# Performance work log

Measured on AMD Instinct MI355X. Metric: run time of the kernel, lower is better.

The kernel has to match this reference:

```python
import jax, jax.numpy as jnp
import numpy as np

D_MODEL = 256
NHEAD = 8
D_K = D_MODEL // NHEAD
IM_SIZE = 8
SCALE = float(IM_SIZE ** 2)  # sqrt(im_size**4)


def setup_inputs() -> dict:
    key = jax.random.key(0)
    ks = jax.random.split(key, 9)
    B, P, S = 8, 256, 8
    s = 1.0 / np.sqrt(D_MODEL)
    return {
        "x": jax.random.normal(ks[0], (B, P, S, S, D_MODEL), jnp.float32),
        "Wq": jax.random.normal(ks[1], (D_MODEL, D_MODEL), jnp.float32) * s,
        "bq": jax.random.normal(ks[2], (D_MODEL,), jnp.float32) * s,
        "Wk": jax.random.normal(ks[3], (D_MODEL, D_MODEL), jnp.float32) * s,
        "bk": jax.random.normal(ks[4], (D_MODEL,), jnp.float32) * s,
        "Wv": jax.random.normal(ks[5], (D_MODEL, D_MODEL), jnp.float32) * s,
        "bv": jax.random.normal(ks[6], (D_MODEL,), jnp.float32) * s,
        "Wo": jax.random.normal(ks[7], (D_MODEL, D_MODEL), jnp.float32) * s,
        "bo": jax.random.normal(ks[8], (D_MODEL,), jnp.float32) * s,
    }


def _split_heads(t):
    # torch: view(..., d_k, nhead).permute(0,5,1,2,3,4) -> [b, n, p, x, y, d_k]
    b, p, sx, sy, _ = t.shape
    t = t.reshape(b, p, sx, sy, D_K, NHEAD)
    return jnp.transpose(t, (0, 5, 1, 2, 3, 4))


def reference(x, Wq, bq, Wk, bk, Wv, bv, Wo, bo):
    Q = _split_heads(x @ Wq.T + bq)
    K = _split_heads(x @ Wk.T + bk)
    V = _split_heads(x @ Wv.T + bv)
    # scores over flattened (x, y, d_k) dims
    scores = jnp.einsum('bnpxyd,bnqxyd->bnpq', Q, K) / SCALE
    attn = jax.nn.softmax(scores, axis=-1)
    out = jnp.einsum('bnpq,bnqxyd->bnpxyd', attn, V)
    # permute to [b, p, x, y, d_k, n] then merge (d_k, n) -> d_model
    out = jnp.transpose(out, (0, 2, 3, 4, 5, 1))
    b, p, sx, sy, _, _ = out.shape
    out = out.reshape(b, p, sx, sy, NHEAD * D_K)
    return out @ Wo.T + bo
```

## Files before the change

### kernel.cpp

```cpp
#include <hip/hip_runtime.h>
#include <hip/hip_bf16.h>


typedef __bf16 bf16;
typedef __attribute__((ext_vector_type(8))) __bf16 bf16x8;
typedef __attribute__((ext_vector_type(4))) float floatx4;
typedef __attribute__((ext_vector_type(8))) unsigned short ushort8;

#define CDIM 2048

static __device__ __forceinline__ floatx4 mfma16(bf16x8 a, bf16x8 b, floatx4 c) {
  return __builtin_amdgcn_mfma_f32_16x16x32_bf16(a, b, c, 0, 0, 0);
}

static __device__ __forceinline__ void gload_lds16(const void* g, void* l) {
  __builtin_amdgcn_global_load_lds((const __attribute__((address_space(1))) void*)g,
                                   (__attribute__((address_space(3))) void*)l, 16, 0, 0);
}

__global__ __launch_bounds__(256) void k0_prep(
    const float* __restrict__ Wq, const float* __restrict__ bq,
    const float* __restrict__ Wk, const float* __restrict__ bk,
    const float* __restrict__ Wv, const float* __restrict__ bv,
    const float* __restrict__ Wo,
    bf16* __restrict__ Wp, bf16* __restrict__ Wk3, float* __restrict__ biasp)
{
  const int bid = blockIdx.x, tid = threadIdx.x;
  int g = (bid & 31) * 256 + tid;
  int lane = g & 63, rowblk = (g >> 6) & 15, kk = g >> 10;
  int h = lane >> 4, cl = lane & 15;
  int d0 = kk * 32 + 8 * h;
  if (bid < 32) {
    int ip = rowblk * 16 + cl;
    int isrc = ((ip & 31) << 3) | (ip >> 5);
#pragma unroll
    for (int mat = 0; mat < 3; mat++) {
      const float* W = (mat == 0) ? Wq : (mat == 1) ? Wk : Wv;
      bf16x8 v;
#pragma unroll
      for (int j = 0; j < 8; j++) v[j] = (bf16)W[isrc * 256 + d0 + j];
      *reinterpret_cast<bf16x8*>(Wp + ((size_t)mat * 8192 + g) * 8) = v;
    }
    if (bid == 0 && tid < 256) {
      int bs = ((tid & 31) << 3) | (tid >> 5);
      biasp[tid] = bq[bs]; biasp[256 + tid] = bk[bs]; biasp[512 + tid] = bv[bs];
    }
  } else {
    int j = rowblk * 16 + cl;
    bf16x8 v;
#pragma unroll
    for (int jj = 0; jj < 8; jj++) {
      int c = d0 + jj;
      v[jj] = (bf16)Wo[j * 256 + (((c & 31) << 3) | (c >> 5))];
    }
    *reinterpret_cast<bf16x8*>(Wk3 + (size_t)g * 8) = v;
  }
}

__global__ __launch_bounds__(512, 4) void k1_qkv(
    const float* __restrict__ x, const bf16* __restrict__ Wp,
    const float* __restrict__ biasp,
    bf16* __restrict__ Qs, bf16* __restrict__ Ks, bf16* __restrict__ Vt)
{
  __shared__ bf16 buf[2][64 * 256];
  const int bx = blockIdx.x;
  const int tid = threadIdx.x;
  const int lane = tid & 63;
  const int w = tid >> 6;
  const int h = lane >> 4, cl = lane & 15;
  const int c7 = cl & 7;

  floatx4 sreg[8];

#define K1_LOAD(VB)                                                          \
  {                                                                          \
    int a_ = (VB) / 24;                                                      \
    int t0_ = (a_ * 8 + ((VB) & 7)) * 64;                                    \
    _Pragma("unroll")                                                        \
    for (int k = 0; k < 4; ++k) {                                            \
      int G = k * 512 + tid;                                                 \
      int row = G >> 5;                                                      \
      const float* sp = x + (size_t)(t0_ + row) * 256 + (G & 31) * 8;        \
      sreg[2 * k]     = *reinterpret_cast<const floatx4*>(sp);               \
      sreg[2 * k + 1] = *reinterpret_cast<const floatx4*>(sp + 4);           \
    }                                                                        \
  }

#define K1_CVTWRITE(BUFI)                                                    \
  {                                                                          \
    _Pragma("unroll")                                                        \
    for (int k = 0; k < 4; ++k) {                                            \
      int G = k * 512 + tid;                                                 \
      int row = G >> 5;                                                      \
      bf16x8 v;                                                              \
      _Pragma("unroll")                                                      \
      for (int j = 0; j < 4; j++) {                                          \
        v[j] = (bf16)sreg[2 * k][j];                                         \
        v[4 + j] = (bf16)sreg[2 * k + 1][j];                                 \
      }                                                                      \
      int Gp = (G & ~7) | ((G ^ row) & 7);                                   \
      *reinterpret_cast<bf16x8*>(&buf[BUFI][Gp * 8]) = v;                    \
    }                                                                        \
  }

#define K1_COMPUTE(VB, BUFI)                                                 \
  {                                                                          \
    int a_ = (VB) / 24;                                                      \
    int rem_ = (VB) - a_ * 24;                                               \
    int mat_ = rem_ >> 3;                                                    \
    int t0_ = (a_ * 8 + (rem_ & 7)) * 64;                                    \
    const bf16* Wm = Wp + (size_t)mat_ * 65536;                              \
    floatx4 acc[4][2];                                                       \
    _Pragma("unroll")                                                        \
    for (int i = 0; i < 4; i++)                                              \
      _Pragma("unroll")                                                      \
      for (int j = 0; j < 2; j++) acc[i][j] = (floatx4)0.0f;                 \
    _Pragma("unroll 2")                                                      \
    for (int kk = 0; kk < 8; ++kk) {                                         \
      bf16x8 av[4];                                                          \
      _Pragma("unroll")                                                      \
      for (int mt = 0; mt < 4; mt++) {                                       \
        int rr = mt * 16 + cl;                                               \
        int G = rr * 32 + kk * 4 + h;                                        \
        int Gp = (G & ~7) | ((G ^ c7) & 7);                                  \
        av[mt] = *reinterpret_cast<const bf16x8*>(&buf[BUFI][Gp * 8]);       \
      }                                                                      \
      bf16x8 b0 = *reinterpret_cast<const bf16x8*>(                          \
          Wm + ((size_t)(kk * 16 + w * 2 + 0) * 64 + lane) * 8);             \
      bf16x8 b1 = *reinterpret_cast<const bf16x8*>(                          \
          Wm + ((size_t)(kk * 16 + w * 2 + 1) * 64 + lane) * 8);             \
      _Pragma("unroll")                                                      \
      for (int mt = 0; mt < 4; mt++) acc[mt][0] = mfma16(av[mt], b0, acc[mt][0]); \
      _Pragma("unroll")                                                      \
      for (int mt = 0; mt < 4; mt++) acc[mt][1] = mfma16(av[mt], b1, acc[mt][1]); \
    }                                                                        \
    int b_ = t0_ >> 14;                                                      \
    int p_ = (t0_ >> 6) & 255;                                               \
    if (mat_ < 2) {                                                          \
      bf16* ob = ((mat_ == 0) ? Qs : Ks) + ((size_t)(b_ * 8 + w) * 256 + p_) * 2048; \
      _Pragma("unroll")                                                      \
      for (int nt = 0; nt < 2; nt++) {                                       \
        const int ip = w * 32 + nt * 16 + cl;                                \
        const float bb = biasp[mat_ * 256 + ip];                             \
        const int dk = nt * 16 + cl;                                         \
        _Pragma("unroll")                                                    \
        for (int mt = 0; mt < 4; mt++)                                       \
          _Pragma("unroll")                                                  \
          for (int r = 0; r < 4; r++) {                                      \
            int sxy = mt * 16 + 4 * h + r;                                   \
            ob[sxy * 32 + dk] = (bf16)(acc[mt][nt][r] + bb);                 \
          }                                                                  \
      }                                                                      \
    } else {                                                                 \
      _Pragma("unroll")                                                      \
      for (int nt = 0; nt < 2; nt++) {                                       \
        const int ip = w * 32 + nt * 16 + cl;                                \
        const float bb = biasp[512 + ip];                                    \
        _Pragma("unroll")                                                    \
        for (int mt = 0; mt < 4; mt++)                                       \
          _Pragma("unroll")                                                  \
          for (int r = 0; r < 4; r++) {                                      \
            int t = t0_ + mt * 16 + 4 * h + r;                               \
            Vt[(size_t)t * 256 + ip] = (bf16)(acc[mt][nt][r] + bb);          \
          }                                                                  \
      }                                                                      \
    }                                                                        \
  }

  K1_LOAD(bx);
  K1_CVTWRITE(0);
  __syncthreads();
#pragma unroll
  for (int u = 1; u < 4; ++u) {
    K1_LOAD(bx + u * 1536);
    K1_COMPUTE(bx + (u - 1) * 1536, (u - 1) & 1);
    __syncthreads();
    K1_CVTWRITE(u & 1);
    __syncthreads();
  }
  K1_COMPUTE(bx + 3 * 1536, 1);

#undef K1_LOAD
#undef K1_CVTWRITE
#undef K1_COMPUTE
}

__global__ __launch_bounds__(1024, 1) void k2a_scores(
    const bf16* __restrict__ Qs, const bf16* __restrict__ Ks,
    bf16* __restrict__ attn)
{
  __shared__ bf16 Qch[3][128 * 64];
  __shared__ bf16 Kch[3][256 * 64];
  __shared__ float redmax[4][4][32];
  __shared__ float redsum[4][4][32];

  const int bx = blockIdx.x;
  const int bn = bx & 63;
  const int p0 = (bx >> 6) * 128;
  const int tid = threadIdx.x;
  const int lane = tid & 63;
  const int w = tid >> 6;
  const int wr = w >> 2, wc = w & 3;
  const int h = lane >> 4, cl = lane & 15;

  const bf16* Qb = Qs + (size_t)bn * 524288 + (size_t)p0 * 2048;
  const bf16* Kb = Ks + (size_t)bn * 524288;

  const int Lq = w * 64 + lane;
  const int rq = Lq >> 3, sq = (Lq & 7) ^ (rq & 7);
  const size_t qsrc = (size_t)rq * 2048 + sq * 8;
  int rk[2]; size_t ksrc[2];
#pragma unroll
  for (int i = 0; i < 2; ++i) {
    int L = i * 1024 + w * 64 + lane;
    rk[i] = L >> 3;
    int s = (L & 7) ^ (rk[i] & 7);
    ksrc[i] = (size_t)rk[i] * 2048 + s * 8;
  }

#define K2A_STAGE(bufi, c)                                                  \
  {                                                                         \
    gload_lds16(Qb + qsrc + (c) * 64, &Qch[bufi][(w * 64) * 8]);            \
    gload_lds16(Kb + ksrc[0] + (c) * 64, &Kch[bufi][(w * 64) * 8]);         \
    gload_lds16(Kb + ksrc[1] + (c) * 64, &Kch[bufi][(1024 + w * 64) * 8]);  \
  }

  floatx4 acc[2][4];
#pragma unroll
  for (int i = 0; i < 2; i++)
#pragma unroll
    for (int j = 0; j < 4; j++) acc[i][j] = (floatx4)0.0f;

  K2A_STAGE(0, 0);
  K2A_STAGE(1, 1);
  asm volatile("s_waitcnt vmcnt(3)" ::: "memory");
  __builtin_amdgcn_s_barrier();
  __builtin_amdgcn_sched_barrier(0);

  for (int c = 0; c < 32; ++c) {
    const int cur = c % 3;
    if (c + 2 < 32) { const int nb = (c + 2) % 3; K2A_STAGE(nb, c + 2); }
#pragma unroll
    for (int kk = 0; kk < 2; ++kk) {
      bf16x8 av[2], bv[4];
#pragma unroll
      for (int mt = 0; mt < 2; mt++) {
        int row = wr * 32 + mt * 16 + cl;
        int gg = kk * 4 + h;
        av[mt] = *reinterpret_cast<const bf16x8*>(
            &Qch[cur][(row * 8 + (gg ^ (row & 7))) * 8]);
      }
#pragma unroll
      for (int nt = 0; nt < 4; nt++) {
        int row = wc * 64 + nt * 16 + cl;
        int gg = kk * 4 + h;
        bv[nt] = *reinterpret_cast<const bf16x8*>(
            &Kch[cur][(row * 8 + (gg ^ (row & 7))) * 8]);
      }
#pragma unroll
      for (int nt = 0; nt < 4; nt++)
#pragma unroll
        for (int mt = 0; mt < 2; mt++)
          acc[mt][nt] = mfma16(av[mt], bv[nt], acc[mt][nt]);
    }
    if (c + 2 < 32) asm volatile("s_waitcnt vmcnt(3)" ::: "memory");
    else            asm volatile("s_waitcnt vmcnt(0)" ::: "memory");
    __builtin_amdgcn_s_barrier();
    __builtin_amdgcn_sched_barrier(0);
  }

  float pm[2][4];
#pragma unroll
  for (int mt = 0; mt < 2; mt++)
#pragma unroll
    for (int r = 0; r < 4; r++)
      pm[mt][r] = fmaxf(fmaxf(acc[mt][0][r], acc[mt][1][r]),
                        fmaxf(acc[mt][2][r], acc[mt][3][r]));
#pragma unroll
  for (int off = 1; off < 16; off <<= 1)
#pragma unroll
    for (int mt = 0; mt < 2; mt++)
#pragma unroll
      for (int r = 0; r < 4; r++)
        pm[mt][r] = fmaxf(pm[mt][r], __shfl_xor(pm[mt][r], off, 64));
  if (cl == 0) {
#pragma unroll
    for (int mt = 0; mt < 2; mt++)
#pragma unroll
      for (int r = 0; r < 4; r++) redmax[wr][wc][mt * 16 + 4 * h + r] = pm[mt][r];
  }
  __syncthreads();

  float gm[2][4], ps[2][4];
#pragma unroll
  for (int mt = 0; mt < 2; mt++)
#pragma unroll
    for (int r = 0; r < 4; r++) {
      int row = mt * 16 + 4 * h + r;
      gm[mt][r] = fmaxf(fmaxf(redmax[wr][0][row], redmax[wr][1][row]),
                        fmaxf(redmax[wr][2][row], redmax[wr][3][row]));
      ps[mt][r] = 0.0f;
    }
  const float KS = 1.44269504088896340736f / 64.0f;
#pragma unroll
  for (int mt = 0; mt < 2; mt++)
#pragma unroll
    for (int nt = 0; nt < 4; nt++)
#pragma unroll
      for (int r = 0; r < 4; r++) {
        float e = exp2f((acc[mt][nt][r] - gm[mt][r]) * KS);
        acc[mt][nt][r] = e;
        ps[mt][r] += e;
      }
#pragma unroll
  for (int off = 1; off < 16; off <<= 1)
#pragma unroll
    for (int mt = 0; mt < 2; mt++)
#pragma unroll
      for (int r = 0; r < 4; r++) ps[mt][r] += __shfl_xor(ps[mt][r], off, 64);
  if (cl == 0) {
#pragma unroll
    for (int mt = 0; mt < 2; mt++)
#pragma unroll
      for (int r = 0; r < 4; r++) redsum[wr][wc][mt * 16 + 4 * h + r] = ps[mt][r];
  }
  __syncthreads();

#pragma unroll
  for (int mt = 0; mt < 2; mt++)
#pragma unroll
    for (int r = 0; r < 4; r++) {
      int row = mt * 16 + 4 * h + r;
      float gs = (redsum[wr][0][row] + redsum[wr][1][row])
               + (redsum[wr][2][row] + redsum[wr][3][row]);
      ps[mt][r] = 1.0f / gs;
    }
#pragma unroll
  for (int nt = 0; nt < 4; nt++) {
    int q = wc * 64 + nt * 16 + cl;
#pragma unroll
    for (int mt = 0; mt < 2; mt++)
#pragma unroll
      for (int r = 0; r < 4; r++) {
        int row = p0 + wr * 32 + mt * 16 + 4 * h + r;
        attn[(size_t)bn * 65536 + row * 256 + q] = (bf16)(acc[mt][nt][r] * ps[mt][r]);
      }
  }
#undef K2A_STAGE
}

__global__ __launch_bounds__(256) void k2t_transpose(
    const bf16* __restrict__ Vtok, bf16* __restrict__ Vq)
{
  const int bx = blockIdx.x;
  const int bn = bx & 63;
  const int r2 = bx >> 6;
  const int q0 = (r2 & 3) * 64;
  const int c0 = (r2 >> 2) * 64;
  const int b = bn >> 3, n = bn & 7;
  __shared__ unsigned short tile[64][65];
  const unsigned short* src = (const unsigned short*)Vtok;
  unsigned short* dst = (unsigned short*)Vq + (size_t)bn * 524288;
  {
    const int q = threadIdx.x >> 3;
    const int cj = (threadIdx.x & 7) * 8;
    const int c = c0 + cj;
    const int sxy = c >> 5, dk0 = c & 31;
#pragma unroll
    for (int it = 0; it < 2; ++it) {
      int qq = q + it * 32;
      size_t sa = (size_t)((b * 256 + q0 + qq) * 64 + sxy) * 256 + n * 32 + dk0;
      ushort8 s = *reinterpret_cast<const ushort8*>(src + sa);
#pragma unroll
      for (int j = 0; j < 8; j++) tile[qq][cj + j] = s[j];
    }
  }
  __syncthreads();
  {
    const int crow = threadIdx.x >> 2;
    const int qj = (threadIdx.x & 3) * 8;
#pragma unroll
    for (int it = 0; it < 2; ++it) {
      int qq = qj + it * 32;
      ushort8 sv;
#pragma unroll
      for (int j = 0; j < 8; j++) sv[j] = tile[qq + j][crow];
      *reinterpret_cast<ushort8*>(dst + (size_t)(c0 + crow) * 256 + q0 + qq) = sv;
    }
  }
}

__global__ __launch_bounds__(512, 6) void k2b_pv(
    const bf16* __restrict__ attn, const bf16* __restrict__ Vq,
    bf16* __restrict__ yhat)
{
  __shared__ bf16 As[64 * 256];
  const int bx = blockIdx.x;
  const int bn = bx & 63;
  const int r2 = bx >> 6;
  const int p0 = (r2 & 3) * 64;
  const int c0 = (r2 >> 2) * 256;
  const int b = bn >> 3, n = bn & 7;
  const int tid = threadIdx.x;
  const int lane = tid & 63;
  const int w = tid >> 6;
  const int h = lane >> 4, cl = lane & 15;
  const int c7 = cl & 7;

  const bf16* Ab = attn + (size_t)bn * 65536 + (size_t)p0 * 256;
  const bf16* Vb = Vq + (size_t)bn * 524288;

#pragma unroll
  for (int i = 0; i < 4; ++i) {
    int L = (i * 8 + w) * 64 + lane;
    int S = (L & ~7) | ((L ^ (L >> 5)) & 7);
    gload_lds16(Ab + (size_t)S * 8, &As[(size_t)(i * 8 + w) * 64 * 8]);
  }
  __syncthreads();

  floatx4 acc[4][2];
#pragma unroll
  for (int i = 0; i < 4; i++)
#pragma unroll
    for (int j = 0; j < 2; j++) acc[i][j] = (floatx4)0.0f;

#pragma unroll 2
  for (int kk = 0; kk < 8; ++kk) {
    bf16x8 av[4];
#pragma unroll
    for (int mt = 0; mt < 4; mt++) {
      int rr = mt * 16 + cl;
      int G = rr * 32 + kk * 4 + h;
      int Gp = (G & ~7) | ((G ^ c7) & 7);
      av[mt] = *reinterpret_cast<const bf16x8*>(&As[Gp * 8]);
    }
    bf16x8 b0 = *reinterpret_cast<const bf16x8*>(
        Vb + (size_t)(c0 + w * 32 + cl) * 256 + kk * 32 + 8 * h);
    bf16x8 b1 = *reinterpret_cast<const bf16x8*>(
        Vb + (size_t)(c0 + w * 32 + 16 + cl) * 256 + kk * 32 + 8 * h);
#pragma unroll
    for (int mt = 0; mt < 4; mt++) acc[mt][0] = mfma16(av[mt], b0, acc[mt][0]);
#pragma unroll
    for (int mt = 0; mt < 4; mt++) acc[mt][1] = mfma16(av[mt], b1, acc[mt][1]);
  }

#pragma unroll
  for (int nt = 0; nt < 2; nt++) {
    const int cg = c0 + w * 32 + nt * 16 + cl;
    const int dk = cg & 31, sxy = cg >> 5;
#pragma unroll
    for (int mt = 0; mt < 4; mt++)
#pragma unroll
      for (int r = 0; r < 4; r++) {
        int p = p0 + mt * 16 + 4 * h + r;
        size_t t = (size_t)((b * 256 + p) * 64) + sxy;
        yhat[t * 256 + n * 32 + dk] = (bf16)acc[mt][nt][r];
      }
  }
}

__global__ __launch_bounds__(512, 6) void k3_out(
    const bf16* __restrict__ yhat, const bf16* __restrict__ Wk3,
    const float* __restrict__ bo, float* __restrict__ outp)
{
  __shared__ bf16 As[64 * 256];
  const int t0 = blockIdx.x * 64;
  const int tid = threadIdx.x;
  const int lane = tid & 63;
  const int w = tid >> 6;
  const int h = lane >> 4, cl = lane & 15;
  const int c7 = cl & 7;

  const bf16* Ab = yhat + (size_t)t0 * 256;

#pragma unroll
  for (int i = 0; i < 4; ++i) {
    int L = (i * 8 + w) * 64 + lane;
    int S = (L & ~7) | ((L ^ (L >> 5)) & 7);
    gload_lds16(Ab + (size_t)S * 8, &As[(size_t)(i * 8 + w) * 64 * 8]);
  }
  __syncthreads();

  floatx4 acc[4][2];
#pragma unroll
  for (int i = 0; i < 4; i++)
#pragma unroll
    for (int j = 0; j < 2; j++) acc[i][j] = (floatx4)0.0f;

#pragma unroll 2
  for (int kk = 0; kk < 8; ++kk) {
    bf16x8 av[4];
#pragma unroll
    for (int mt = 0; mt < 4; mt++) {
      int rr = mt * 16 + cl;
      int G = rr * 32 + kk * 4 + h;
      int Gp = (G & ~7) | ((G ^ c7) & 7);
      av[mt] = *reinterpret_cast<const bf16x8*>(&As[Gp * 8]);
    }
    bf16x8 b0 = *reinterpret_cast<const bf16x8*>(
        Wk3 + ((size_t)(kk * 16 + w * 2 + 0) * 64 + lane) * 8);
    bf16x8 b1 = *reinterpret_cast<const bf16x8*>(
        Wk3 + ((size_t)(kk * 16 + w * 2 + 1) * 64 + lane) * 8);
#pragma unroll
    for (int mt = 0; mt < 4; mt++) acc[mt][0] = mfma16(av[mt], b0, acc[mt][0]);
#pragma unroll
    for (int mt = 0; mt < 4; mt++) acc[mt][1] = mfma16(av[mt], b1, acc[mt][1]);
  }

#pragma unroll
  for (int nt = 0; nt < 2; nt++) {
    const int j = w * 32 + nt * 16 + cl;
    const float bb = bo[j];
#pragma unroll
    for (int mt = 0; mt < 4; mt++)
#pragma unroll
      for (int r = 0; r < 4; r++)
        outp[(size_t)(t0 + mt * 16 + 4 * h + r) * 256 + j] = acc[mt][nt][r] + bb;
  }
}

extern "C" void kernel_launch(void* const* d_in, const int* in_sizes, int n_in,
                              void* d_out, int out_size, void* d_ws, size_t ws_size,
                              hipStream_t stream) {
  const float* x  = (const float*)d_in[0];
  const float* Wq = (const float*)d_in[1];
  const float* bq = (const float*)d_in[2];
  const float* Wk = (const float*)d_in[3];
  const float* bk = (const float*)d_in[4];
  const float* Wv = (const float*)d_in[5];
  const float* bv = (const float*)d_in[6];
  const float* Wo = (const float*)d_in[7];
  const float* bo = (const float*)d_in[8];
  float* outp = (float*)d_out;

  char* ws = (char*)d_ws;
  const size_t SZ_QKV = 67108864;
  size_t off = 0;
  bf16* Qs   = (bf16*)(ws + off); off += SZ_QKV;
  bf16* Ks   = (bf16*)(ws + off); off += SZ_QKV;
  bf16* Vtok = (bf16*)(ws + off); off += SZ_QKV;
  bf16* attn = (bf16*)(ws + off); off += 8388608;
  bf16* Wp   = (bf16*)(ws + off); off += 393216;
  bf16* Wk3  = (bf16*)(ws + off); off += 131072;
  float* biasp = (float*)(ws + off); off += 3072;
  if (ws_size < off) return;

  bf16* yhat = Qs;
  bf16* Vq   = Ks;

  k0_prep<<<64, 256, 0, stream>>>(Wq, bq, Wk, bk, Wv, bv, Wo, Wp, Wk3, biasp);
  k1_qkv<<<1536, 512, 0, stream>>>(x, Wp, biasp, Qs, Ks, Vtok);
  k2a_scores<<<128, 1024, 0, stream>>>(Qs, Ks, attn);
  k2t_transpose<<<8192, 256, 0, stream>>>(Vtok, Vq);
  k2b_pv<<<2048, 512, 0, stream>>>(attn, Vq, yhat);
  k3_out<<<2048, 512, 0, stream>>>(yhat, Wk3, bo, outp);
}
```

Baseline: 313.1 us.

## Pin QKV weight slice in registers per block and split output columns across blocks

The QKV projection kernel now fixes each block to one projection matrix and one half of its output columns. The block's weight fragments are preloaded into registers once and reused for all four token tiles, so the inner loop no longer fetches weights from global memory at every k-step. The grid doubles to 3072 blocks and each wave computes one 16-column tile instead of two. In exchange, each x tile is now read and converted by six blocks instead of three, which leans on L2 hits to absorb the extra input traffic.

After: 328.7 us. 1.05x slower.

```diff
diff --git a/kernel.cpp b/kernel.cpp
--- a/kernel.cpp
+++ b/kernel.cpp
@@ -64,23 +64,38 @@
 {
   __shared__ bf16 buf[2][64 * 256];
   const int bx = blockIdx.x;
+  const int a0 = bx / 48;
+  const int rem = bx - a0 * 48;
+  const int mat = rem >> 4;
+  const int ch = (rem >> 3) & 1;
+  const int x8 = rem & 7;
   const int tid = threadIdx.x;
   const int lane = tid & 63;
   const int w = tid >> 6;
   const int h = lane >> 4, cl = lane & 15;
   const int c7 = cl & 7;
 
+  const bf16* Wm = Wp + (size_t)mat * 65536;
+  bf16x8 wreg[8];
+#pragma unroll
+  for (int kk = 0; kk < 8; ++kk)
+    wreg[kk] = *reinterpret_cast<const bf16x8*>(
+        Wm + ((size_t)(kk * 16 + ch * 8 + w) * 64 + lane) * 8);
+
+  const int ip = (ch * 8 + w) * 16 + cl;
+  const float bb = biasp[mat * 256 + ip];
+  const int n_ = ip >> 5, dkc = ip & 31;
+  bf16* qkout = (mat == 0) ? Qs : Ks;
+
   floatx4 sreg[8];
 
-#define K1_LOAD(VB)                                                          \
+#define K1_LOAD(T0)                                                          \
   {                                                                          \
-    int a_ = (VB) / 24;                                                      \
-    int t0_ = (a_ * 8 + ((VB) & 7)) * 64;                                    \
     _Pragma("unroll")                                                        \
     for (int k = 0; k < 4; ++k) {                                            \
       int G = k * 512 + tid;                                                 \
       int row = G >> 5;                                                      \
-      const float* sp = x + (size_t)(t0_ + row) * 256 + (G & 31) * 8;        \
+      const float* sp = x + (size_t)((T0) + row) * 256 + (G & 31) * 8;       \
       sreg[2 * k]     = *reinterpret_cast<const floatx4*>(sp);               \
       sreg[2 * k + 1] = *reinterpret_cast<const floatx4*>(sp + 4);           \
     }                                                                        \
@@ -103,19 +118,12 @@
     }                                                                        \
   }
 
-#define K1_COMPUTE(VB, BUFI)                                                 \
+#define K1_COMPUTE(T0, BUFI)                                                 \
   {                                                                          \
-    int a_ = (VB) / 24;                                                      \
-    int rem_ = (VB) - a_ * 24;                                               \
-    int mat_ = rem_ >> 3;                                                    \
-    int t0_ = (a_ * 8 + (rem_ & 7)) * 64;                                    \
-    const bf16* Wm = Wp + (size_t)mat_ * 65536;                              \
-    floatx4 acc[4][2];                                                       \
+    floatx4 acc[4];                                                          \
     _Pragma("unroll")                                                        \
-    for (int i = 0; i < 4; i++)                                              \
-      _Pragma("unroll")                                                      \
-      for (int j = 0; j < 2; j++) acc[i][j] = (floatx4)0.0f;                 \
-    _Pragma("unroll 2")                                                      \
+    for (int i = 0; i < 4; i++) acc[i] = (floatx4)0.0f;                      \
+    _Pragma("unroll")                                                        \
     for (int kk = 0; kk < 8; ++kk) {                                         \
       bf16x8 av[4];                                                          \
       _Pragma("unroll")                                                      \
@@ -125,60 +133,48 @@
         int Gp = (G & ~7) | ((G ^ c7) & 7);                                  \
         av[mt] = *reinterpret_cast<const bf16x8*>(&buf[BUFI][Gp * 8]);       \
       }                                                                      \
-      bf16x8 b0 = *reinterpret_cast<const bf16x8*>(                          \
-          Wm + ((size_t)(kk * 16 + w * 2 + 0) * 64 + lane) * 8);             \
-      bf16x8 b1 = *reinterpret_cast<const bf16x8*>(                          \
-          Wm + ((size_t)(kk * 16 + w * 2 + 1) * 64 + lane) * 8);             \
       _Pragma("unroll")                                                      \
-      for (int mt = 0; mt < 4; mt++) acc[mt][0] = mfma16(av[mt], b0, acc[mt][0]); \
+      for (int mt = 0; mt < 4; mt++)                                         \
+        acc[mt] = mfma16(av[mt], wreg[kk], acc[mt]);                         \
+    }                                                                        \
+    int b_ = (T0) >> 14;                                                     \
+    int p_ = ((T0) >> 6) & 255;                                              \
+    if (mat < 2) {                                                           \
+      bf16* ob = qkout + ((size_t)(b_ * 8 + n_) * 256 + p_) * 2048;          \
       _Pragma("unroll")                                                      \
-      for (int mt = 0; mt < 4; mt++) acc[mt][1] = mfma16(av[mt], b1, acc[mt][1]); \
-    }                                                                        \
-    int b_ = t0_ >> 14;                                                      \
-    int p_ = (t0_ >> 6) & 255;                                               \
-    if (mat_ < 2) {                                                          \
-      bf16* ob = ((mat_ == 0) ? Qs : Ks) + ((size_t)(b_ * 8 + w) * 256 + p_) * 2048; \
-      _Pragma("unroll")                                                      \
-      for (int nt = 0; nt < 2; nt++) {                                       \
-        const int ip = w * 32 + nt * 16 + cl;                                \
-        const float bb = biasp[mat_ * 256 + ip];                             \
-        const int dk = nt * 16 + cl;                                         \
+      for (int mt = 0; mt < 4; mt++)                                         \
         _Pragma("unroll")                                                    \
-        for (int mt = 0; mt < 4; mt++)                                       \
-          _Pragma("unroll")                                                  \
-          for (int r = 0; r < 4; r++) {                                      \
-            int sxy = mt * 16 + 4 * h + r;                                   \
-            ob[sxy * 32 + dk] = (bf16)(acc[mt][nt][r] + bb);                 \
-          }                                                                  \
-      }                                                                      \
+        for (int r = 0; r < 4; r++) {                                        \
+          int sxy = mt * 16 + 4 * h + r;                                     \
+          ob[sxy * 32 + dkc] = (bf16)(acc[mt][r] + bb);                      \
+        }                                                                    \
     } else {                                                                 \
       _Pragma("unroll")                                                      \
-      for (int nt = 0; nt < 2; nt++) {                                       \
-        const int ip = w * 32 + nt * 16 + cl;                                \
-        const float bb = biasp[512 + ip];                                    \
+      for (int mt = 0; mt < 4; mt++)                                         \
         _Pragma("unroll")                                                    \
-        for (int mt = 0; mt < 4; mt++)                                       \
-          _Pragma("unroll")                                                  \
-          for (int r = 0; r < 4; r++) {                                      \
-            int t = t0_ + mt * 16 + 4 * h + r;                               \
-            Vt[(size_t)t * 256 + ip] = (bf16)(acc[mt][nt][r] + bb);          \
-          }                                                                  \
-      }                                                                      \
+        for (int r = 0; r < 4; r++) {                                        \
+          int t = (T0) + mt * 16 + 4 * h + r;                                \
+          Vt[(size_t)t * 256 + ip] = (bf16)(acc[mt][r] + bb);                \
+        }                                                                    \
     }                                                                        \
   }
 
-  K1_LOAD(bx);
+  int t0 = ((a0 + 0 * 64) * 8 + x8) * 64;
+  K1_LOAD(t0);
   K1_CVTWRITE(0);
   __syncthreads();
 #pragma unroll
   for (int u = 1; u < 4; ++u) {
-    K1_LOAD(bx + u * 1536);
-    K1_COMPUTE(bx + (u - 1) * 1536, (u - 1) & 1);
+    int t0n = ((a0 + u * 64) * 8 + x8) * 64;
+    int t0p = ((a0 + (u - 1) * 64) * 8 + x8) * 64;
+    K1_LOAD(t0n);
+    K1_COMPUTE(t0p, (u - 1) & 1);
     __syncthreads();
     K1_CVTWRITE(u & 1);
     __syncthreads();
   }
-  K1_COMPUTE(bx + 3 * 1536, 1);
+  int t0l = ((a0 + 3 * 64) * 8 + x8) * 64;
+  K1_COMPUTE(t0l, 1);
 
 #undef K1_LOAD
 #undef K1_CVTWRITE
@@ -549,7 +545,7 @@
   bf16* Vq   = Ks;
 
   k0_prep<<<64, 256, 0, stream>>>(Wq, bq, Wk, bk, Wv, bv, Wo, Wp, Wk3, biasp);
-  k1_qkv<<<1536, 512, 0, stream>>>(x, Wp, biasp, Qs, Ks, Vtok);
+  k1_qkv<<<3072, 512, 0, stream>>>(x, Wp, biasp, Qs, Ks, Vtok);
   k2a_scores<<<128, 1024, 0, stream>>>(Qs, Ks, attn);
   k2t_transpose<<<8192, 256, 0, stream>>>(Vtok, Vq);
   k2b_pv<<<2048, 512, 0, stream>>>(attn, Vq, yhat);
```

## Fuse V transpose into QKV projection epilogue via LDS staging

Applied to the files above, without the earlier changes.

The QKV projection kernel now tiles tokens by (batch, spatial position, block of 64 patches) rather than by contiguous tokens. The V output can then be transposed through shared memory and written directly in the [b,n,(sxy,dk),p] layout the PV kernel consumes. This removes the separate transpose kernel and its full 64 MB read and write round trip of V. In exchange, the x loads become strided (one 1 KB row per patch), Q/K stores scatter across patches, and extra LDS passes and barriers are added to the pipelined loop.

After: 344.8 us. +10.1%, slower.

```diff
diff --git a/kernel.cpp b/kernel.cpp
--- a/kernel.cpp
+++ b/kernel.cpp
@@ -60,7 +60,7 @@
 __global__ __launch_bounds__(512, 4) void k1_qkv(
     const float* __restrict__ x, const bf16* __restrict__ Wp,
     const float* __restrict__ biasp,
-    bf16* __restrict__ Qs, bf16* __restrict__ Ks, bf16* __restrict__ Vt)
+    bf16* __restrict__ Qs, bf16* __restrict__ Ks, bf16* __restrict__ Vq)
 {
   __shared__ bf16 buf[2][64 * 256];
   const int bx = blockIdx.x;
@@ -71,16 +71,25 @@
   const int c7 = cl & 7;
 
   floatx4 sreg[8];
+  floatx4 acc[4][2];
+
+#define K1_DEC(VB)                                                           \
+    int a_ = (VB) / 24;                                                      \
+    int rem_ = (VB) - a_ * 24;                                               \
+    int mat_ = rem_ >> 3;                                                    \
+    int tile_ = a_ * 8 + (rem_ & 7);                                         \
+    int b_ = tile_ >> 8, sxy_ = (tile_ >> 2) & 63, pblk_ = tile_ & 3;        \
+    (void)mat_; (void)b_; (void)sxy_; (void)pblk_;
 
 #define K1_LOAD(VB)                                                          \
   {                                                                          \
-    int a_ = (VB) / 24;                                                      \
-    int t0_ = (a_ * 8 + ((VB) & 7)) * 64;                                    \
+    K1_DEC(VB)                                                               \
     _Pragma("unroll")                                                        \
     for (int k = 0; k < 4; ++k) {                                            \
       int G = k * 512 + tid;                                                 \
       int row = G >> 5;                                                      \
-      const float* sp = x + (size_t)(t0_ + row) * 256 + (G & 31) * 8;        \
+      const float* sp = x +                                                  \
+          (size_t)((b_ * 256 + pblk_ * 64 + row) * 64 + sxy_) * 256 + (G & 31) * 8; \
       sreg[2 * k]     = *reinterpret_cast<const floatx4*>(sp);               \
       sreg[2 * k + 1] = *reinterpret_cast<const floatx4*>(sp + 4);           \
     }                                                                        \
@@ -105,12 +114,8 @@
 
 #define K1_COMPUTE(VB, BUFI)                                                 \
   {                                                                          \
-    int a_ = (VB) / 24;                                                      \
-    int rem_ = (VB) - a_ * 24;                                               \
-    int mat_ = rem_ >> 3;                                                    \
-    int t0_ = (a_ * 8 + (rem_ & 7)) * 64;                                    \
+    K1_DEC(VB)                                                               \
     const bf16* Wm = Wp + (size_t)mat_ * 65536;                              \
-    floatx4 acc[4][2];                                                       \
     _Pragma("unroll")                                                        \
     for (int i = 0; i < 4; i++)                                              \
       _Pragma("unroll")                                                      \
@@ -134,35 +139,58 @@
       _Pragma("unroll")                                                      \
       for (int mt = 0; mt < 4; mt++) acc[mt][1] = mfma16(av[mt], b1, acc[mt][1]); \
     }                                                                        \
-    int b_ = t0_ >> 14;                                                      \
-    int p_ = (t0_ >> 6) & 255;                                               \
     if (mat_ < 2) {                                                          \
-      bf16* ob = ((mat_ == 0) ? Qs : Ks) + ((size_t)(b_ * 8 + w) * 256 + p_) * 2048; \
+      bf16* ob = ((mat_ == 0) ? Qs : Ks) + (size_t)(b_ * 8 + w) * 524288;    \
       _Pragma("unroll")                                                      \
       for (int nt = 0; nt < 2; nt++) {                                       \
-        const int ip = w * 32 + nt * 16 + cl;                                \
-        const float bb = biasp[mat_ * 256 + ip];                             \
+        const float bb = biasp[mat_ * 256 + w * 32 + nt * 16 + cl];          \
         const int dk = nt * 16 + cl;                                         \
         _Pragma("unroll")                                                    \
         for (int mt = 0; mt < 4; mt++)                                       \
           _Pragma("unroll")                                                  \
           for (int r = 0; r < 4; r++) {                                      \
-            int sxy = mt * 16 + 4 * h + r;                                   \
-            ob[sxy * 32 + dk] = (bf16)(acc[mt][nt][r] + bb);                 \
+            int pl = mt * 16 + 4 * h + r;                                    \
+            ob[(size_t)(pblk_ * 64 + pl) * 2048 + sxy_ * 32 + dk]            \
+                = (bf16)(acc[mt][nt][r] + bb);                               \
           }                                                                  \
       }                                                                      \
-    } else {                                                                 \
+    }                                                                        \
+  }
+
+#define K1_V_EPI_LDS(VB, BUFI)                                               \
+  {                                                                          \
+    K1_DEC(VB)                                                               \
+    if (mat_ == 2) {                                                         \
       _Pragma("unroll")                                                      \
       for (int nt = 0; nt < 2; nt++) {                                       \
         const int ip = w * 32 + nt * 16 + cl;                                \
         const float bb = biasp[512 + ip];                                    \
+        const int sx = 8 * (ip & 7);                                         \
         _Pragma("unroll")                                                    \
         for (int mt = 0; mt < 4; mt++)                                       \
           _Pragma("unroll")                                                  \
           for (int r = 0; r < 4; r++) {                                      \
-            int t = t0_ + mt * 16 + 4 * h + r;                               \
-            Vt[(size_t)t * 256 + ip] = (bf16)(acc[mt][nt][r] + bb);          \
+            int pl = mt * 16 + 4 * h + r;                                    \
+            buf[BUFI][ip * 64 + (pl ^ sx)] = (bf16)(acc[mt][nt][r] + bb);    \
           }                                                                  \
+      }                                                                      \
+    }                                                                        \
+  }
+
+#define K1_V_EPI_STORE(VB, BUFI)                                             \
+  {                                                                          \
+    K1_DEC(VB)                                                               \
+    if (mat_ == 2) {                                                         \
+      _Pragma("unroll")                                                      \
+      for (int j = 0; j < 4; ++j) {                                          \
+        int ip_ = j * 64 + (tid >> 3);                                       \
+        int c8 = tid & 7;                                                    \
+        int pb = c8 ^ (ip_ & 7);                                             \
+        ushort8 v = *reinterpret_cast<const ushort8*>(                       \
+            &buf[BUFI][ip_ * 64 + pb * 8]);                                  \
+        int n_ = ip_ >> 5, dk_ = ip_ & 31;                                   \
+        *reinterpret_cast<ushort8*>(Vq + (size_t)(b_ * 8 + n_) * 524288      \
+            + (size_t)(sxy_ * 32 + dk_) * 256 + pblk_ * 64 + c8 * 8) = v;    \
       }                                                                      \
     }                                                                        \
   }
@@ -175,14 +203,23 @@
     K1_LOAD(bx + u * 1536);
     K1_COMPUTE(bx + (u - 1) * 1536, (u - 1) & 1);
     __syncthreads();
+    K1_V_EPI_LDS(bx + (u - 1) * 1536, (u - 1) & 1);
     K1_CVTWRITE(u & 1);
     __syncthreads();
+    K1_V_EPI_STORE(bx + (u - 1) * 1536, (u - 1) & 1);
   }
   K1_COMPUTE(bx + 3 * 1536, 1);
-
+  __syncthreads();
+  K1_V_EPI_LDS(bx + 3 * 1536, 1);
+  __syncthreads();
+  K1_V_EPI_STORE(bx + 3 * 1536, 1);
+
+#undef K1_DEC
 #undef K1_LOAD
 #undef K1_CVTWRITE
 #undef K1_COMPUTE
+#undef K1_V_EPI_LDS
+#undef K1_V_EPI_STORE
 }
 
 __global__ __launch_bounds__(1024, 1) void k2a_scores(
@@ -347,47 +384,6 @@
       }
   }
 #undef K2A_STAGE
-}
-
-__global__ __launch_bounds__(256) void k2t_transpose(
-    const bf16* __restrict__ Vtok, bf16* __restrict__ Vq)
-{
-  const int bx = blockIdx.x;
-  const int bn = bx & 63;
-  const int r2 = bx >> 6;
-  const int q0 = (r2 & 3) * 64;
-  const int c0 = (r2 >> 2) * 64;
-  const int b = bn >> 3, n = bn & 7;
-  __shared__ unsigned short tile[64][65];
-  const unsigned short* src = (const unsigned short*)Vtok;
-  unsigned short* dst = (unsigned short*)Vq + (size_t)bn * 524288;
-  {
-    const int q = threadIdx.x >> 3;
-    const int cj = (threadIdx.x & 7) * 8;
-    const int c = c0 + cj;
-    const int sxy = c >> 5, dk0 = c & 31;
-#pragma unroll
-    for (int it = 0; it < 2; ++it) {
-      int qq = q + it * 32;
-      size_t sa = (size_t)((b * 256 + q0 + qq) * 64 + sxy) * 256 + n * 32 + dk0;
-      ushort8 s = *reinterpret_cast<const ushort8*>(src + sa);
-#pragma unroll
-      for (int j = 0; j < 8; j++) tile[qq][cj + j] = s[j];
-    }
-  }
-  __syncthreads();
-  {
-    const int crow = threadIdx.x >> 2;
-    const int qj = (threadIdx.x & 3) * 8;
-#pragma unroll
-    for (int it = 0; it < 2; ++it) {
-      int qq = qj + it * 32;
-      ushort8 sv;
-#pragma unroll
-      for (int j = 0; j < 8; j++) sv[j] = tile[qq + j][crow];
-      *reinterpret_cast<ushort8*>(dst + (size_t)(c0 + crow) * 256 + q0 + qq) = sv;
-    }
-  }
 }
 
 __global__ __launch_bounds__(512, 6) void k2b_pv(
@@ -538,7 +534,7 @@
   size_t off = 0;
   bf16* Qs   = (bf16*)(ws + off); off += SZ_QKV;
   bf16* Ks   = (bf16*)(ws + off); off += SZ_QKV;
-  bf16* Vtok = (bf16*)(ws + off); off += SZ_QKV;
+  bf16* Vq   = (bf16*)(ws + off); off += SZ_QKV;
   bf16* attn = (bf16*)(ws + off); off += 8388608;
   bf16* Wp   = (bf16*)(ws + off); off += 393216;
   bf16* Wk3  = (bf16*)(ws + off); off += 131072;
@@ -546,12 +542,10 @@
   if (ws_size < off) return;
 
   bf16* yhat = Qs;
-  bf16* Vq   = Ks;
 
   k0_prep<<<64, 256, 0, stream>>>(Wq, bq, Wk, bk, Wv, bv, Wo, Wp, Wk3, biasp);
-  k1_qkv<<<1536, 512, 0, stream>>>(x, Wp, biasp, Qs, Ks, Vtok);
+  k1_qkv<<<1536, 512, 0, stream>>>(x, Wp, biasp, Qs, Ks, Vq);
   k2a_scores<<<128, 1024, 0, stream>>>(Qs, Ks, attn);
-  k2t_transpose<<<8192, 256, 0, stream>>>(Vtok, Vq);
   k2b_pv<<<2048, 512, 0, stream>>>(attn, Vq, yhat);
   k3_out<<<2048, 512, 0, stream>>>(yhat, Wk3, bo, outp);
 }
```
